# Performance work log

Measured on AMD Instinct MI355X. Metric: run time of the kernel, lower is better.

## Reference

```python
import jax, jax.numpy as jnp
import numpy as np

N = 100000
E = 1600000
D_IN = 128
D_H = 128


def setup_inputs() -> dict:
    key = jax.random.key(0)
    ks = jax.random.split(key, 8)
    x = jax.random.normal(ks[0], (N, D_IN), dtype=jnp.float32)
    edge_index = jax.random.randint(ks[1], (2, E), 0, N, dtype=jnp.int64)
    edge_weights = jax.random.uniform(ks[2], (E,), dtype=jnp.float32)
    # GCNConv params (glorot-ish scale), bias zeros like PyG default init reset
    W1 = jax.random.normal(ks[3], (D_IN, D_H), dtype=jnp.float32) / np.sqrt(D_IN)
    b1 = jnp.zeros((D_H,), dtype=jnp.float32)
    W2 = jax.random.normal(ks[4], (D_H, D_H), dtype=jnp.float32) / np.sqrt(D_H)
    b2 = jnp.zeros((D_H,), dtype=jnp.float32)
    a_prelu = jnp.full((D_H,), 0.25, dtype=jnp.float32)  # nn.PReLU(hidden_dim)
    return {"x": x, "edge_index": edge_index, "edge_weights": edge_weights,
            "W1": W1, "b1": b1, "W2": W2, "b2": b2, "a_prelu": a_prelu}


def _gcn_norm(edge_index, edge_weights, n_nodes):
    # add self loops (weight 1), symmetric normalization deg^-1/2 A deg^-1/2
    loop = jnp.arange(n_nodes, dtype=edge_index.dtype)
    src = jnp.concatenate([edge_index[0], loop])
    dst = jnp.concatenate([edge_index[1], loop])
    w = jnp.concatenate([edge_weights, jnp.ones((n_nodes,), edge_weights.dtype)])
    deg = jax.ops.segment_sum(w, dst, num_segments=n_nodes)
    dis = jnp.where(deg > 0, jax.lax.rsqrt(jnp.maximum(deg, 1e-12)), 0.0)
    norm = dis[src] * w * dis[dst]
    return src, dst, norm


def _gcn_layer(h, W, b, src, dst, norm, n_nodes):
    h = h @ W                                   # [N, D] linear (no bias)
    msg = h[src] * norm[:, None]                # gather + scale  [E+N, D]
    out = jax.ops.segment_sum(msg, dst, num_segments=n_nodes)
    return out + b


def _prelu(z, a):
    return jnp.where(z >= 0, z, a * z)


def reference(x, edge_index, edge_weights, W1, b1, W2, b2, a_prelu):
    n = x.shape[0]
    src, dst, norm = _gcn_norm(edge_index, edge_weights, n)
    z = _prelu(_gcn_layer(x, W1, b1, src, dst, norm, n), a_prelu)
    z = _prelu(_gcn_layer(z, W2, b2, src, dst, norm, n), a_prelu)
    return z
```

## Files before the change

### kernel.cpp

```cpp
#include <hip/hip_runtime.h>
#include <hip/hip_fp16.h>

#define D 128
#define CAP 64
#define NBKT 512
#define CHUNK 4096
#define BKTCAP 5120

typedef _Float16 f16x8 __attribute__((ext_vector_type(8)));
typedef float f32x4 __attribute__((ext_vector_type(4)));

__global__ __launch_bounds__(256) void k_bin(const int* __restrict__ ei,
        const float* __restrict__ ew, int* __restrict__ gcur,
        int2* __restrict__ gbkt, int e) {
    __shared__ int hist[NBKT];
    __shared__ int base[NBKT];
    int t = threadIdx.x;
    int b0 = blockIdx.x * CHUNK;
    int cnt = min(CHUNK, e - b0);
    for (int i = t; i < NBKT; i += 256) hist[i] = 0;
    __syncthreads();
    int meta[16]; float w[16]; int pos[16]; int bkt[16];
    #pragma unroll
    for (int j = 0; j < 16; ++j) {
        int li = t + j * 256;
        bkt[j] = -1;
        if (li < cnt) {
            int i = b0 + li;
            int d = ei[e + i];
            int s = ei[i];
            bkt[j] = d >> 8;
            meta[j] = s | ((d & 255) << 24);
            w[j] = ew[i];
            pos[j] = atomicAdd(&hist[bkt[j]], 1);
        }
    }
    __syncthreads();
    for (int i = t; i < NBKT; i += 256)
        if (hist[i] > 0) base[i] = atomicAdd(&gcur[i], hist[i]);
    __syncthreads();
    #pragma unroll
    for (int j = 0; j < 16; ++j) {
        if (bkt[j] >= 0) {
            int idx = base[bkt[j]] + pos[j];
            if (idx < BKTCAP)
                gbkt[(size_t)bkt[j] * BKTCAP + idx] =
                    make_int2(meta[j], __float_as_int(w[j]));
        }
    }
}

__global__ __launch_bounds__(1024) void k_scat2(const int2* __restrict__ gbkt,
        const int* __restrict__ gcur, const float2* __restrict__ X,
        int2* __restrict__ slot, int* __restrict__ rsc, float* __restrict__ dis,
        __half2* __restrict__ xh, int n) {
    __shared__ int cur[256];
    __shared__ float wsum[256];
    __shared__ float disv[256];
    int bkt = blockIdx.x;
    int nodebase = bkt << 8;
    int t = threadIdx.x;
    int cnt = min(gcur[bkt], BKTCAP);
    if (t < 256) { cur[t] = 0; wsum[t] = 0.f; }
    __syncthreads();
    for (int i = t; i < cnt; i += 1024) {
        int2 r = gbkt[(size_t)bkt * BKTCAP + i];
        int dl = (unsigned)r.x >> 24;
        int pos = atomicAdd(&cur[dl], 1);
        atomicAdd(&wsum[dl], __int_as_float(r.y));
        if (pos < CAP)
            slot[(((size_t)(nodebase + dl)) << 6) + pos] =
                make_int2(r.x & 0xFFFFFF, r.y);
    }
    __syncthreads();
    if (t < 256) {
        int v = nodebase + t;
        float dv = 1.f;
        if (v < n) {
            dv = rsqrtf(1.0f + wsum[t]);
            dis[v] = dv;
            rsc[v] = cur[t];
        }
        disv[t] = dv;
    }
    __syncthreads();
    int nrow = min(256, n - nodebase);
    size_t rowbase = (size_t)nodebase << 6;
    for (int idx = t; idx < nrow * 64; idx += 1024) {
        float dv2 = disv[idx >> 6];
        float2 f = X[rowbase + idx];
        xh[rowbase + idx] = __floats2half2_rn(dv2 * f.x, dv2 * f.y);
    }
}

__global__ __launch_bounds__(256) void k_agg(const __half2* __restrict__ Hs,
        const int2* __restrict__ slot, const int* __restrict__ rsc,
        const float* __restrict__ dis, __half2* __restrict__ out, int n) {
    int wid = threadIdx.x >> 6, lane = threadIdx.x & 63;
    int v = blockIdx.x * 4 + wid;
    if (v >= n) return;
    int half = lane >> 5;
    int m = lane & 31;
    int c = min(rsc[v], 62);
    int c1 = c + 1;
    const int2* row = slot + ((size_t)v << 6);
    const __half* Hb = (const __half*)Hs;

    float4 acc = make_float4(0.f, 0.f, 0.f, 0.f);
    for (int i = 0; i < c1; i += 8) {
        int2 e[4];
        #pragma unroll
        for (int k = 0; k < 4; ++k) {
            int j = i + 2 * k + half;
            int jj = j - 1;
            jj = (jj < 0) ? 0 : (jj >= CAP ? CAP - 1 : jj);
            int2 ld = row[jj];
            bool real = (j >= 1) && (j < c1);
            int2 ee;
            ee.x = real ? ld.x : v;
            ee.y = real ? ld.y : ((j == 0) ? 0x3f800000 : 0);
            e[k] = ee;
        }
        float2 g[4];
        #pragma unroll
        for (int k = 0; k < 4; ++k)
            g[k] = *(const float2*)(Hb + ((size_t)e[k].x << 7) + (m << 2));
        #pragma unroll
        for (int k = 0; k < 4; ++k) {
            float w = __int_as_float(e[k].y);
            union { float2 f; __half2 h[2]; } u; u.f = g[k];
            float2 lo = __half22float2(u.h[0]);
            float2 hi = __half22float2(u.h[1]);
            acc.x = fmaf(w, lo.x, acc.x);
            acc.y = fmaf(w, lo.y, acc.y);
            acc.z = fmaf(w, hi.x, acc.z);
            acc.w = fmaf(w, hi.y, acc.w);
        }
    }
    acc.x += __shfl_xor(acc.x, 32);
    acc.y += __shfl_xor(acc.y, 32);
    acc.z += __shfl_xor(acc.z, 32);
    acc.w += __shfl_xor(acc.w, 32);
    if (half == 0) {
        float dv = dis[v];
        union { float2 f; __half2 h[2]; } o;
        o.h[0] = __floats2half2_rn(dv * acc.x, dv * acc.y);
        o.h[1] = __floats2half2_rn(dv * acc.z, dv * acc.w);
        *(float2*)((__half*)out + ((size_t)v << 7) + (m << 2)) = o.f;
    }
}

__global__ __launch_bounds__(256) void k_packW(const float* __restrict__ W1,
        const float* __restrict__ W2, __half* __restrict__ Wpk1,
        __half* __restrict__ Wpk2) {
    int gidx = blockIdx.x * 256 + threadIdx.x;
    if (gidx >= 4096) return;
    const float* W = (gidx < 2048) ? W1 : W2;
    __half* P = (gidx < 2048) ? Wpk1 : Wpk2;
    int idx = gidx & 2047;
    int lane = idx & 63, nt = (idx >> 6) & 7, ks = idx >> 9;
    int col = nt * 16 + (lane & 15);
    int kb = ks * 32 + (lane >> 4) * 8;
    #pragma unroll
    for (int j = 0; j < 8; ++j)
        P[idx * 8 + j] = __float2half(W[(kb + j) * D + col]);
}

template <bool HALF_OUT>
__global__ __launch_bounds__(256) void k_gemm(const __half* __restrict__ A,
        const __half* __restrict__ Wpk, const float* __restrict__ b,
        const float* __restrict__ ap, const float* __restrict__ dis,
        void* __restrict__ Cv, int n) {
    int t = threadIdx.x;
    int wv = t >> 6, lane = t & 63;
    int base = blockIdx.x * 64 + wv * 16;
    int row = base + (lane & 15);
    int rowc = min(row, n - 1);
    int kg = lane >> 4;

    const f16x8* Arow = (const f16x8*)(A + (size_t)rowc * D);
    f16x8 afr[4];
    #pragma unroll
    for (int ks = 0; ks < 4; ++ks) afr[ks] = Arow[ks * 4 + kg];

    const f16x8* Wp = (const f16x8*)Wpk;
    f32x4 acc[8];
    #pragma unroll
    for (int nt = 0; nt < 8; ++nt) acc[nt] = (f32x4){0.f, 0.f, 0.f, 0.f};

    #pragma unroll
    for (int ks = 0; ks < 4; ++ks) {
        #pragma unroll
        for (int nt = 0; nt < 8; ++nt) {
            f16x8 bfr = Wp[(ks * 8 + nt) * 64 + lane];
            acc[nt] = __builtin_amdgcn_mfma_f32_16x16x32_f16(afr[ks], bfr, acc[nt], 0, 0, 0);
        }
    }

    int c0 = lane & 15;
    int r0 = base + (lane >> 4) * 4;
    float dv[4];
    #pragma unroll
    for (int q = 0; q < 4; ++q)
        dv[q] = HALF_OUT ? dis[min(r0 + q, n - 1)] : 1.0f;
    #pragma unroll
    for (int nt = 0; nt < 8; ++nt) {
        int col = nt * 16 + c0;
        float bb = b[col], aa = ap[col];
        #pragma unroll
        for (int q = 0; q < 4; ++q) {
            int r = r0 + q;
            if (r < n) {
                float z = acc[nt][q] + bb;
                z = (z >= 0.f) ? z : aa * z;
                if (HALF_OUT) ((__half*)Cv)[(size_t)r * D + col] = __float2half(dv[q] * z);
                else          ((float*)Cv)[(size_t)r * D + col] = z;
            }
        }
    }
}


extern "C" void kernel_launch(void* const* d_in, const int* in_sizes, int n_in,
                              void* d_out, int out_size, void* d_ws, size_t ws_size,
                              hipStream_t stream) {
    const float* x  = (const float*)d_in[0];
    const int*   ei = (const int*)d_in[1];
    const float* ew = (const float*)d_in[2];
    const float* W1 = (const float*)d_in[3];
    const float* b1 = (const float*)d_in[4];
    const float* W2 = (const float*)d_in[5];
    const float* b2 = (const float*)d_in[6];
    const float* ap = (const float*)d_in[7];

    int n = in_sizes[0] / D;
    int e = in_sizes[2];

    int*     gcur = (int*)d_ws;
    float*   dis  = (float*)(gcur + NBKT);
    int*     rsc  = (int*)(dis + n);
    int2*    gbkt = (int2*)(rsc + n);
    int2*    slot = gbkt + (size_t)NBKT * BKTCAP;
    __half2* xh   = (__half2*)(slot + (size_t)n * CAP);
    __half2* z1h  = xh + (size_t)n * 64;
    __half2* ah   = z1h + (size_t)n * 64;
    __half*  Wpk1 = (__half*)(ah + (size_t)n * 64);
    __half*  Wpk2 = Wpk1 + 16384;
    float*   out  = (float*)d_out;

    int nbin = (e + CHUNK - 1) / CHUNK;
    int nbb  = (n + 255) / 256;
    int nbw  = (n + 3) / 4;
    int nbg  = (n + 63) / 64;

    hipMemsetAsync(gcur, 0, NBKT * sizeof(int), stream);
    k_packW<<<16, 256, 0, stream>>>(W1, W2, Wpk1, Wpk2);
    k_bin<<<nbin, 256, 0, stream>>>(ei, ew, gcur, gbkt, e);
    k_scat2<<<nbb, 1024, 0, stream>>>(gbkt, gcur, (const float2*)x, slot, rsc, dis, xh, n);

    k_agg<<<nbw, 256, 0, stream>>>(xh, slot, rsc, dis, ah, n);
    k_gemm<true><<<nbg, 256, 0, stream>>>((const __half*)ah, Wpk1, b1, ap, dis, (void*)z1h, n);
    k_agg<<<nbw, 256, 0, stream>>>(z1h, slot, rsc, dis, ah, n);
    k_gemm<false><<<nbg, 256, 0, stream>>>((const __half*)ah, Wpk2, b2, ap, dis, (void*)out, n);
}
```

Before: 242.4 us.

## Widen aggregation gathers to 16-byte loads with shuffled edge metadata

```diff
diff --git a/kernel.cpp b/kernel.cpp
--- a/kernel.cpp
+++ b/kernel.cpp
@@ -99,54 +99,47 @@
     int wid = threadIdx.x >> 6, lane = threadIdx.x & 63;
     int v = blockIdx.x * 4 + wid;
     if (v >= n) return;
-    int half = lane >> 5;
-    int m = lane & 31;
+    int eslot = lane >> 4;
+    int dg = lane & 15;
     int c = min(rsc[v], 62);
     int c1 = c + 1;
     const int2* row = slot + ((size_t)v << 6);
-    const __half* Hb = (const __half*)Hs;
-
-    float4 acc = make_float4(0.f, 0.f, 0.f, 0.f);
-    for (int i = 0; i < c1; i += 8) {
-        int2 e[4];
-        #pragma unroll
-        for (int k = 0; k < 4; ++k) {
-            int j = i + 2 * k + half;
-            int jj = j - 1;
-            jj = (jj < 0) ? 0 : (jj >= CAP ? CAP - 1 : jj);
-            int2 ld = row[jj];
-            bool real = (j >= 1) && (j < c1);
-            int2 ee;
-            ee.x = real ? ld.x : v;
-            ee.y = real ? ld.y : ((j == 0) ? 0x3f800000 : 0);
-            e[k] = ee;
-        }
-        float2 g[4];
-        #pragma unroll
-        for (int k = 0; k < 4; ++k)
-            g[k] = *(const float2*)(Hb + ((size_t)e[k].x << 7) + (m << 2));
-        #pragma unroll
-        for (int k = 0; k < 4; ++k) {
-            float w = __int_as_float(e[k].y);
-            union { float2 f; __half2 h[2]; } u; u.f = g[k];
-            float2 lo = __half22float2(u.h[0]);
-            float2 hi = __half22float2(u.h[1]);
-            acc.x = fmaf(w, lo.x, acc.x);
-            acc.y = fmaf(w, lo.y, acc.y);
-            acc.z = fmaf(w, hi.x, acc.z);
-            acc.w = fmaf(w, hi.y, acc.w);
-        }
-    }
-    acc.x += __shfl_xor(acc.x, 32);
-    acc.y += __shfl_xor(acc.y, 32);
-    acc.z += __shfl_xor(acc.z, 32);
-    acc.w += __shfl_xor(acc.w, 32);
-    if (half == 0) {
+    const char* Hc = (const char*)Hs;
+
+    int2 mm;
+    if (lane == 0) mm = make_int2(v, 0x3f800000);
+    else if (lane < c1) mm = row[lane - 1];
+    else mm = make_int2(v, 0);
+    int voff = mm.x << 8;
+    float wf = __int_as_float(mm.y);
+
+    float acc[8];
+    #pragma unroll
+    for (int d = 0; d < 8; ++d) acc[d] = 0.f;
+
+    for (int j0 = 0; j0 < c1; j0 += 8) {
+        int sl0 = j0 + eslot, sl1 = j0 + 4 + eslot;
+        int vo0 = __shfl(voff, sl0); float w0 = __shfl(wf, sl0);
+        int vo1 = __shfl(voff, sl1); float w1 = __shfl(wf, sl1);
+        f16x8 g0 = *(const f16x8*)(Hc + vo0 + (dg << 4));
+        f16x8 g1 = *(const f16x8*)(Hc + vo1 + (dg << 4));
+        #pragma unroll
+        for (int d = 0; d < 8; ++d) acc[d] = fmaf(w0, (float)g0[d], acc[d]);
+        #pragma unroll
+        for (int d = 0; d < 8; ++d) acc[d] = fmaf(w1, (float)g1[d], acc[d]);
+    }
+    #pragma unroll
+    for (int d = 0; d < 8; ++d) {
+        acc[d] += __shfl_xor(acc[d], 16);
+        acc[d] += __shfl_xor(acc[d], 32);
+    }
+    if (eslot == 0) {
         float dv = dis[v];
-        union { float2 f; __half2 h[2]; } o;
-        o.h[0] = __floats2half2_rn(dv * acc.x, dv * acc.y);
-        o.h[1] = __floats2half2_rn(dv * acc.z, dv * acc.w);
-        *(float2*)((__half*)out + ((size_t)v << 7) + (m << 2)) = o.f;
+        union { f16x8 v8; __half2 h[4]; } o;
+        #pragma unroll
+        for (int d = 0; d < 4; ++d)
+            o.h[d] = __floats2half2_rn(dv * acc[2 * d], dv * acc[2 * d + 1]);
+        *(f16x8*)((char*)out + ((size_t)v << 8) + (dg << 4)) = o.v8;
     }
 }
 
```

Result: faster. 229.5 us (-5.3%).
